# Optimization experiments

Measured on AMD Instinct MI355X. Metric: run time of the kernel, lower is better.

## Reference

```python
import jax, jax.numpy as jnp
import numpy as np

B, C, D = 524288, 256, 128


def setup_inputs() -> dict:
    key = jax.random.key(0)
    ks = jax.random.split(key, 20)
    s = 1.0 / np.sqrt(D)
    w = lambda k, shp: jax.random.normal(k, shp, dtype=jnp.float32) * s
    return {
        "h": jax.random.normal(ks[0], (B, D), dtype=jnp.float32),
        "g": jax.random.normal(ks[1], (C, D), dtype=jnp.float32),
        "cluster_id": jax.random.randint(ks[2], (B,), 0, C, dtype=jnp.int32),
        "Wq": w(ks[3], (D, D)),
        "Wk": w(ks[4], (D, D)),
        "attn_bias": jax.random.uniform(ks[5], (D,), dtype=jnp.float32, minval=-0.1, maxval=0.1),
        "Ws_w": w(ks[6], (1, D)),
        "Ws_b": jnp.zeros((1,), dtype=jnp.float32),
        "W_w": w(ks[7], (D, D)),
        "W_b": jnp.zeros((D,), dtype=jnp.float32),
        "Fs_w": w(ks[8], (D, D)),
        "Fs_b": jnp.zeros((D,), dtype=jnp.float32),
        "H1_w": w(ks[9], (D, D)),
        "H1_b": jnp.zeros((D,), dtype=jnp.float32),
        "G1_w": w(ks[10], (D, D)),
        "G1_b": jnp.zeros((D,), dtype=jnp.float32),
        "H2_w": w(ks[11], (D, D)),
        "H2_b": jnp.zeros((D,), dtype=jnp.float32),
        "G2_w": w(ks[12], (D, D)),
        "G2_b": jnp.zeros((D,), dtype=jnp.float32),
    }


def reference(h, g, cluster_id, Wq, Wk, attn_bias, Ws_w, Ws_b, W_w, W_b,
              Fs_w, Fs_b, H1_w, H1_b, G1_w, G1_b, H2_w, H2_b, G2_w, G2_b):
    # --- GNTransmitterUnit: virtual -> graph node message ---
    g_trans = jnp.tanh(g @ Fs_w.T + Fs_b)                 # (C, D)
    g_n = g_trans[cluster_id]                              # gather per node: (B, D)
    # --- gn_merge (WarpGateUnit with gather): gated mix into node features ---
    z1 = jax.nn.sigmoid(h @ H1_w.T + H1_b + g_n @ G1_w.T + G1_b)
    h_merged = (1.0 - z1) * h + z1 * g_n                   # (B, D)
    # --- VNTransmitterUnit: segmented additive (Bahdanau) attention per cluster ---
    q = g @ Wq.T                                           # (C, D)
    k = h @ Wk.T                                           # (B, D)
    score = jnp.tanh(k + q[cluster_id] + attn_bias) @ Ws_w[0] + Ws_b[0]  # (B,)
    m = jax.ops.segment_max(score, cluster_id, num_segments=C)
    m = jnp.where(jnp.isfinite(m), m, 0.0)                 # guard empty clusters
    e = jnp.exp(score - m[cluster_id])
    denom = jax.ops.segment_sum(e, cluster_id, num_segments=C)
    attn = e / jnp.maximum(denom, 1e-20)[cluster_id]       # segment softmax (B,)
    ctx = jax.ops.segment_sum(attn[:, None] * h, cluster_id, num_segments=C)  # (C, D)
    h_trans = jnp.tanh(ctx @ W_w.T + W_b)                  # (C, D)
    # --- vn_merge (WarpGateUnit): gated mix into virtual-node features ---
    z2 = jax.nn.sigmoid(g @ H2_w.T + H2_b + h_trans @ G2_w.T + G2_b)
    g_merged = (1.0 - z2) * g + z2 * h_trans               # (C, D)
    return jnp.concatenate([h_merged, g_merged], axis=0)   # (B + C, D)
```

## Files before the change

### kernel.cpp

```cpp
#include <hip/hip_runtime.h>
#include <hip/hip_bf16.h>

#define NB   524288
#define NC   256
#define ND   128

typedef __attribute__((ext_vector_type(4))) float f32x4;
typedef __attribute__((ext_vector_type(8))) short bf16x8;

__device__ inline float fast_exp(float x)  { return exp2f(x * 1.4426950408889634f); }
__device__ inline float fast_sigmoid(float x) { return __builtin_amdgcn_rcpf(1.f + fast_exp(-x)); }
__device__ inline float fast_tanh(float x) { return 1.f - 2.f * __builtin_amdgcn_rcpf(1.f + fast_exp(2.f * x)); }

__device__ inline unsigned short f2bf(float f) {
    unsigned u = __float_as_uint(f);
    u += 0x7FFFu + ((u >> 16) & 1u);
    return (unsigned short)(u >> 16);
}

__device__ inline bf16x8 pack8(const float* __restrict__ p) {
    float4 a = *(const float4*)p;
    float4 b = *(const float4*)(p + 4);
    bf16x8 r;
    r[0] = (short)f2bf(a.x); r[1] = (short)f2bf(a.y);
    r[2] = (short)f2bf(a.z); r[3] = (short)f2bf(a.w);
    r[4] = (short)f2bf(b.x); r[5] = (short)f2bf(b.y);
    r[6] = (short)f2bf(b.z); r[7] = (short)f2bf(b.w);
    return r;
}

__device__ inline unsigned enc_f32(float s) {
    unsigned b = __float_as_uint(s);
    return b ^ (unsigned)(((int)b >> 31) | (int)0x80000000);
}

__global__ __launch_bounds__(128) void k1_cluster_prep(
    const float* __restrict__ g, const float* __restrict__ Wq,
    const float* __restrict__ attn_bias,
    const float* __restrict__ Fs_w, const float* __restrict__ Fs_b,
    const float* __restrict__ G1_w, const float* __restrict__ G1_b,
    float* __restrict__ g_trans, float* __restrict__ gG1, float* __restrict__ qb) {
    const int c = blockIdx.x, d = threadIdx.x;
    __shared__ float g_lds[ND];
    __shared__ float gt_lds[ND];
    g_lds[d] = g[c * ND + d];
    __syncthreads();
    float accF = Fs_b[d], accQ = attn_bias[d];
    const float* fr = Fs_w + d * ND;
    const float* qr = Wq + d * ND;
    for (int k = 0; k < ND; ++k) {
        float gv = g_lds[k];
        accF += fr[k] * gv;
        accQ += qr[k] * gv;
    }
    float gt = fast_tanh(accF);
    g_trans[c * ND + d] = gt;
    gt_lds[d] = gt;
    qb[c * ND + d] = accQ;
    __syncthreads();
    float accG = G1_b[d];
    const float* gr = G1_w + d * ND;
    for (int k = 0; k < ND; ++k) accG += gr[k] * gt_lds[k];
    gG1[c * ND + d] = accG;
}

__global__ __launch_bounds__(256) void k2_pass1(
    const float* __restrict__ h, const int* __restrict__ cid,
    const float* __restrict__ Wk, const float* __restrict__ H1w,
    const float* __restrict__ H1b, const float* __restrict__ Wsw,
    const float* __restrict__ Wsb, const float* __restrict__ g_trans,
    const float* __restrict__ gG1, const float* __restrict__ qb,
    float* __restrict__ outh, float* __restrict__ score) {
    __shared__ float k_lds[16][132];
    __shared__ float h1_lds[16][132];
    const int tid = threadIdx.x;
    const int w = tid >> 6, l = tid & 63;
    const int l15 = l & 15, lg = l >> 4;

    bf16x8 bk[2][4], bh[2][4];
#pragma unroll
    for (int t2 = 0; t2 < 2; ++t2) {
        const int trow = (w + t2 * 4) * 16 + l15;
#pragma unroll
        for (int c = 0; c < 4; ++c) {
            const int col = c * 32 + lg * 8;
            bk[t2][c] = pack8(Wk + trow * ND + col);
            bh[t2][c] = pack8(H1w + trow * ND + col);
        }
    }
    const float Wsb0 = Wsb[0];
    const int nb0 = blockIdx.x * 256;

    for (int it = 0; it < 16; ++it) {
        const int nb = nb0 + it * 16;
        bf16x8 af[4];
        const float* hrow = h + (size_t)(nb + l15) * ND + lg * 8;
#pragma unroll
        for (int c = 0; c < 4; ++c) af[c] = pack8(hrow + c * 32);

        f32x4 acck0 = {0.f, 0.f, 0.f, 0.f}, acck1 = {0.f, 0.f, 0.f, 0.f};
        f32x4 acch0 = {0.f, 0.f, 0.f, 0.f}, acch1 = {0.f, 0.f, 0.f, 0.f};
#pragma unroll
        for (int c = 0; c < 4; ++c) {
            acck0 = __builtin_amdgcn_mfma_f32_16x16x32_bf16(af[c], bk[0][c], acck0, 0, 0, 0);
            acck1 = __builtin_amdgcn_mfma_f32_16x16x32_bf16(af[c], bk[1][c], acck1, 0, 0, 0);
            acch0 = __builtin_amdgcn_mfma_f32_16x16x32_bf16(af[c], bh[0][c], acch0, 0, 0, 0);
            acch1 = __builtin_amdgcn_mfma_f32_16x16x32_bf16(af[c], bh[1][c], acch1, 0, 0, 0);
        }
        {
            const int d0 = w * 16 + l15, d1 = (w + 4) * 16 + l15;
#pragma unroll
            for (int r = 0; r < 4; ++r) {
                const int nrow = lg * 4 + r;
                k_lds[nrow][d0] = acck0[r];
                k_lds[nrow][d1] = acck1[r];
                h1_lds[nrow][d0] = acch0[r];
                h1_lds[nrow][d1] = acch1[r];
            }
        }
        __syncthreads();
#pragma unroll
        for (int ni = 0; ni < 4; ++ni) {
            const int n = w * 4 + ni;
            const int node = nb + n;
            const int cc = cid[node];
            float2 kv  = *(const float2*)&k_lds[n][2 * l];
            float2 h1v = *(const float2*)&h1_lds[n][2 * l];
            float2 qv  = *(const float2*)(qb + cc * ND + 2 * l);
            float2 ggv = *(const float2*)(gG1 + cc * ND + 2 * l);
            float2 gtv = *(const float2*)(g_trans + cc * ND + 2 * l);
            float2 hv  = *(const float2*)(h + (size_t)node * ND + 2 * l);
            float2 hbv = *(const float2*)(H1b + 2 * l);
            float2 wsv = *(const float2*)(Wsw + 2 * l);
            float sp = fast_tanh(kv.x + qv.x) * wsv.x + fast_tanh(kv.y + qv.y) * wsv.y;
#pragma unroll
            for (int off = 32; off; off >>= 1) sp += __shfl_xor(sp, off, 64);
            if (l == 0) score[node] = sp + Wsb0;
            float z0 = fast_sigmoid(h1v.x + hbv.x + ggv.x);
            float z1 = fast_sigmoid(h1v.y + hbv.y + ggv.y);
            float2 o = {(1.f - z0) * hv.x + z0 * gtv.x,
                        (1.f - z1) * hv.y + z1 * gtv.y};
            *(float2*)(outh + (size_t)node * ND + 2 * l) = o;
        }
        __syncthreads();
    }
}

__global__ __launch_bounds__(256) void k3_segmax(
    const float* __restrict__ score, const int* __restrict__ cid,
    unsigned* __restrict__ m_enc) {
    __shared__ unsigned mloc[NC];
    const int t = threadIdx.x;
    mloc[t] = 0u;
    __syncthreads();
    for (int i = blockIdx.x * 256 + t; i < NB; i += 256 * 256) {
        atomicMax(&mloc[cid[i]], enc_f32(score[i]));
    }
    __syncthreads();
    atomicMax(m_enc + t, mloc[t]);
}

__global__ __launch_bounds__(256) void k4_pass2(
    const float* __restrict__ h, const int* __restrict__ cid,
    const float* __restrict__ score, const unsigned* __restrict__ m_enc,
    float* __restrict__ ctx_raw, float* __restrict__ denom) {
    __shared__ float cloc[NC * 64];
    __shared__ float dloc[NC];
    __shared__ float mloc[NC];
    const int t = threadIdx.x, w = t >> 6, l = t & 63;
    const int half = blockIdx.x & 1, bg = blockIdx.x >> 1;
    for (int i = t; i < NC * 64; i += 256) cloc[i] = 0.f;
    dloc[t] = 0.f;
    {
        unsigned u = m_enc[t];
        unsigned bits = (u & 0x80000000u) ? (u ^ 0x80000000u) : ~u;
        float f = __uint_as_float(bits);
        mloc[t] = ((bits & 0x7F800000u) == 0x7F800000u) ? 0.f : f;
    }
    __syncthreads();
    const int n0 = bg * 2048 + w * 512;
    const float* hcol = h + half * 64 + l;
    for (int nn = 0; nn < 512; nn += 4) {
        const int n = n0 + nn;
        float4 sc = *(const float4*)(score + n);
        int4 c4 = *(const int4*)(cid + n);
        float e0 = fast_exp(sc.x - mloc[c4.x]);
        float e1 = fast_exp(sc.y - mloc[c4.y]);
        float e2 = fast_exp(sc.z - mloc[c4.z]);
        float e3 = fast_exp(sc.w - mloc[c4.w]);
        float h0 = hcol[(size_t)n * ND];
        float h1 = hcol[(size_t)(n + 1) * ND];
        float h2 = hcol[(size_t)(n + 2) * ND];
        float h3 = hcol[(size_t)(n + 3) * ND];
        atomicAdd(&cloc[c4.x * 64 + l], e0 * h0);
        atomicAdd(&cloc[c4.y * 64 + l], e1 * h1);
        atomicAdd(&cloc[c4.z * 64 + l], e2 * h2);
        atomicAdd(&cloc[c4.w * 64 + l], e3 * h3);
        if (l == 0 && half == 0) {
            atomicAdd(&dloc[c4.x], e0);
            atomicAdd(&dloc[c4.y], e1);
            atomicAdd(&dloc[c4.z], e2);
            atomicAdd(&dloc[c4.w], e3);
        }
    }
    __syncthreads();
    for (int i = t; i < NC * 64; i += 256) {
        const int c = i >> 6;
        unsafeAtomicAdd(&ctx_raw[c * ND + half * 64 + (i & 63)], cloc[i]);
    }
    if (half == 0) unsafeAtomicAdd(&denom[t], dloc[t]);
}

__global__ __launch_bounds__(128) void k5_final(
    const float* __restrict__ g, const float* __restrict__ ctx_raw,
    const float* __restrict__ denom,
    const float* __restrict__ W_w, const float* __restrict__ W_b,
    const float* __restrict__ H2_w, const float* __restrict__ H2_b,
    const float* __restrict__ G2_w, const float* __restrict__ G2_b,
    float* __restrict__ out_g) {
    const int c = blockIdx.x, d = threadIdx.x;
    __shared__ float ctx_l[ND], ht_l[ND], g_l[ND];
    float den = fmaxf(denom[c], 1e-20f);
    float ctxv = ctx_raw[c * ND + d] / den;
    ctx_l[d] = ctxv;
    g_l[d] = g[c * ND + d];
    __syncthreads();
    float acc = W_b[d];
    const float* wr = W_w + d * ND;
    for (int k = 0; k < ND; ++k) acc += wr[k] * ctx_l[k];
    float ht = fast_tanh(acc);
    ht_l[d] = ht;
    __syncthreads();
    float acc2 = H2_b[d] + G2_b[d];
    const float* h2r = H2_w + d * ND;
    const float* g2r = G2_w + d * ND;
    for (int k = 0; k < ND; ++k) acc2 += h2r[k] * g_l[k] + g2r[k] * ht_l[k];
    float z = fast_sigmoid(acc2);
    out_g[c * ND + d] = (1.f - z) * g_l[d] + z * ht;
}

extern "C" void kernel_launch(void* const* d_in, const int* in_sizes, int n_in,
                              void* d_out, int out_size, void* d_ws, size_t ws_size,
                              hipStream_t stream) {
    const float* h        = (const float*)d_in[0];
    const float* g        = (const float*)d_in[1];
    const int*   cid      = (const int*)d_in[2];
    const float* Wq       = (const float*)d_in[3];
    const float* Wk       = (const float*)d_in[4];
    const float* attnb    = (const float*)d_in[5];
    const float* Ws_w     = (const float*)d_in[6];
    const float* Ws_b     = (const float*)d_in[7];
    const float* W_w      = (const float*)d_in[8];
    const float* W_b      = (const float*)d_in[9];
    const float* Fs_w     = (const float*)d_in[10];
    const float* Fs_b     = (const float*)d_in[11];
    const float* H1_w     = (const float*)d_in[12];
    const float* H1_b     = (const float*)d_in[13];
    const float* G1_w     = (const float*)d_in[14];
    const float* G1_b     = (const float*)d_in[15];
    const float* H2_w     = (const float*)d_in[16];
    const float* H2_b     = (const float*)d_in[17];
    const float* G2_w     = (const float*)d_in[18];
    const float* G2_b     = (const float*)d_in[19];
    float* out = (float*)d_out;
    float* ws  = (float*)d_ws;

    float*    g_trans = ws;
    float*    gG1     = ws + 32768;
    float*    qb      = ws + 65536;
    float*    score   = ws + 98304;
    unsigned* m_enc   = (unsigned*)(ws + 622592);
    float*    denom   = ws + 622848;
    float*    ctx_raw = ws + 623104;
    hipMemsetAsync(ws + 622592, 0, (256 + 256 + 32768) * sizeof(float), stream);

    k1_cluster_prep<<<NC, ND, 0, stream>>>(g, Wq, attnb, Fs_w, Fs_b, G1_w, G1_b,
                                           g_trans, gG1, qb);
    k2_pass1<<<2048, 256, 0, stream>>>(h, cid, Wk, H1_w, H1_b, Ws_w, Ws_b,
                                       g_trans, gG1, qb, out, score);
    k3_segmax<<<256, 256, 0, stream>>>(score, cid, m_enc);
    k4_pass2<<<512, 256, 0, stream>>>(h, cid, score, m_enc, ctx_raw, denom);
    k5_final<<<NC, ND, 0, stream>>>(g, ctx_raw, denom, W_w, W_b,
                                    H2_w, H2_b, G2_w, G2_b,
                                    out + (size_t)NB * ND);
}
```

Measured before the change: 1.101 ms.

## Epilogue directly from MFMA registers in pass1; quarter-column vectorized segment accumulation

The pass-1 kernel drops the LDS staging and block barriers and computes the score and gate epilogue straight from the MFMA accumulator layout. The score is reduced over 16 lanes and combined with atomic adds into a pre-zeroed score buffer, which requires extending the memset. Ws_b is dropped from the score because a constant shift cancels in the softmax. The pass-2 kernel splits columns into quarters with padded LDS (stride 33), float4 loads of h and 1024 blocks, to cut LDS usage and improve coalescing. The trade-offs are strided, non-vectorized global loads and stores in the epilogue and extra global atomics on score.

```diff
diff --git a/kernel.cpp b/kernel.cpp
--- a/kernel.cpp
+++ b/kernel.cpp
@@ -68,11 +68,9 @@
     const float* __restrict__ h, const int* __restrict__ cid,
     const float* __restrict__ Wk, const float* __restrict__ H1w,
     const float* __restrict__ H1b, const float* __restrict__ Wsw,
-    const float* __restrict__ Wsb, const float* __restrict__ g_trans,
-    const float* __restrict__ gG1, const float* __restrict__ qb,
+    const float* __restrict__ g_trans, const float* __restrict__ gG1,
+    const float* __restrict__ qb,
     float* __restrict__ outh, float* __restrict__ score) {
-    __shared__ float k_lds[16][132];
-    __shared__ float h1_lds[16][132];
     const int tid = threadIdx.x;
     const int w = tid >> 6, l = tid & 63;
     const int l15 = l & 15, lg = l >> 4;
@@ -88,7 +86,10 @@
             bh[t2][c] = pack8(H1w + trow * ND + col);
         }
     }
-    const float Wsb0 = Wsb[0];
+    const int d0 = w * 16 + l15, d1 = d0 + 64;
+    const float ws0 = Wsw[d0], ws1 = Wsw[d1];
+    const float hb0 = H1b[d0], hb1 = H1b[d1];
+
     const int nb0 = blockIdx.x * 256;
 
     for (int it = 0; it < 16; ++it) {
@@ -107,42 +108,29 @@
             acch0 = __builtin_amdgcn_mfma_f32_16x16x32_bf16(af[c], bh[0][c], acch0, 0, 0, 0);
             acch1 = __builtin_amdgcn_mfma_f32_16x16x32_bf16(af[c], bh[1][c], acch1, 0, 0, 0);
         }
-        {
-            const int d0 = w * 16 + l15, d1 = (w + 4) * 16 + l15;
-#pragma unroll
-            for (int r = 0; r < 4; ++r) {
-                const int nrow = lg * 4 + r;
-                k_lds[nrow][d0] = acck0[r];
-                k_lds[nrow][d1] = acck1[r];
-                h1_lds[nrow][d0] = acch0[r];
-                h1_lds[nrow][d1] = acch1[r];
-            }
+#pragma unroll
+        for (int r = 0; r < 4; ++r) {
+            const int node = nb + lg * 4 + r;
+            const int cc = cid[node];
+            const float* qrow = qb + cc * ND;
+            const float* grow = gG1 + cc * ND;
+            const float* trow = g_trans + cc * ND;
+            const float* hrw  = h + (size_t)node * ND;
+            float q0  = qrow[d0], q1  = qrow[d1];
+            float gg0 = grow[d0], gg1 = grow[d1];
+            float gt0 = trow[d0], gt1 = trow[d1];
+            float hv0 = hrw[d0],  hv1 = hrw[d1];
+            float sp = fast_tanh(acck0[r] + q0) * ws0 + fast_tanh(acck1[r] + q1) * ws1;
+            sp += __shfl_xor(sp, 1);
+            sp += __shfl_xor(sp, 2);
+            sp += __shfl_xor(sp, 4);
+            sp += __shfl_xor(sp, 8);
+            if (l15 == 0) unsafeAtomicAdd(&score[node], sp);
+            float z0 = fast_sigmoid(acch0[r] + hb0 + gg0);
+            float z1 = fast_sigmoid(acch1[r] + hb1 + gg1);
+            outh[(size_t)node * ND + d0] = (1.f - z0) * hv0 + z0 * gt0;
+            outh[(size_t)node * ND + d1] = (1.f - z1) * hv1 + z1 * gt1;
         }
-        __syncthreads();
-#pragma unroll
-        for (int ni = 0; ni < 4; ++ni) {
-            const int n = w * 4 + ni;
-            const int node = nb + n;
-            const int cc = cid[node];
-            float2 kv  = *(const float2*)&k_lds[n][2 * l];
-            float2 h1v = *(const float2*)&h1_lds[n][2 * l];
-            float2 qv  = *(const float2*)(qb + cc * ND + 2 * l);
-            float2 ggv = *(const float2*)(gG1 + cc * ND + 2 * l);
-            float2 gtv = *(const float2*)(g_trans + cc * ND + 2 * l);
-            float2 hv  = *(const float2*)(h + (size_t)node * ND + 2 * l);
-            float2 hbv = *(const float2*)(H1b + 2 * l);
-            float2 wsv = *(const float2*)(Wsw + 2 * l);
-            float sp = fast_tanh(kv.x + qv.x) * wsv.x + fast_tanh(kv.y + qv.y) * wsv.y;
-#pragma unroll
-            for (int off = 32; off; off >>= 1) sp += __shfl_xor(sp, off, 64);
-            if (l == 0) score[node] = sp + Wsb0;
-            float z0 = fast_sigmoid(h1v.x + hbv.x + ggv.x);
-            float z1 = fast_sigmoid(h1v.y + hbv.y + ggv.y);
-            float2 o = {(1.f - z0) * hv.x + z0 * gtv.x,
-                        (1.f - z1) * hv.y + z1 * gtv.y};
-            *(float2*)(outh + (size_t)node * ND + 2 * l) = o;
-        }
-        __syncthreads();
     }
 }
 
@@ -164,12 +152,13 @@
     const float* __restrict__ h, const int* __restrict__ cid,
     const float* __restrict__ score, const unsigned* __restrict__ m_enc,
     float* __restrict__ ctx_raw, float* __restrict__ denom) {
-    __shared__ float cloc[NC * 64];
+    __shared__ float cloc[NC * 33];
     __shared__ float dloc[NC];
     __shared__ float mloc[NC];
     const int t = threadIdx.x, w = t >> 6, l = t & 63;
-    const int half = blockIdx.x & 1, bg = blockIdx.x >> 1;
-    for (int i = t; i < NC * 64; i += 256) cloc[i] = 0.f;
+    const int q = blockIdx.x & 3;
+    const int bg = blockIdx.x >> 2;
+    for (int i = t; i < NC * 33; i += 256) cloc[i] = 0.f;
     dloc[t] = 0.f;
     {
         unsigned u = m_enc[t];
@@ -178,37 +167,27 @@
         mloc[t] = ((bits & 0x7F800000u) == 0x7F800000u) ? 0.f : f;
     }
     __syncthreads();
+    const int colbase = q * 32 + (l & 7) * 4;
     const int n0 = bg * 2048 + w * 512;
-    const float* hcol = h + half * 64 + l;
-    for (int nn = 0; nn < 512; nn += 4) {
-        const int n = n0 + nn;
-        float4 sc = *(const float4*)(score + n);
-        int4 c4 = *(const int4*)(cid + n);
-        float e0 = fast_exp(sc.x - mloc[c4.x]);
-        float e1 = fast_exp(sc.y - mloc[c4.y]);
-        float e2 = fast_exp(sc.z - mloc[c4.z]);
-        float e3 = fast_exp(sc.w - mloc[c4.w]);
-        float h0 = hcol[(size_t)n * ND];
-        float h1 = hcol[(size_t)(n + 1) * ND];
-        float h2 = hcol[(size_t)(n + 2) * ND];
-        float h3 = hcol[(size_t)(n + 3) * ND];
-        atomicAdd(&cloc[c4.x * 64 + l], e0 * h0);
-        atomicAdd(&cloc[c4.y * 64 + l], e1 * h1);
-        atomicAdd(&cloc[c4.z * 64 + l], e2 * h2);
-        atomicAdd(&cloc[c4.w * 64 + l], e3 * h3);
-        if (l == 0 && half == 0) {
-            atomicAdd(&dloc[c4.x], e0);
-            atomicAdd(&dloc[c4.y], e1);
-            atomicAdd(&dloc[c4.z], e2);
-            atomicAdd(&dloc[c4.w], e3);
-        }
-    }
-    __syncthreads();
-    for (int i = t; i < NC * 64; i += 256) {
-        const int c = i >> 6;
-        unsafeAtomicAdd(&ctx_raw[c * ND + half * 64 + (i & 63)], cloc[i]);
-    }
-    if (half == 0) unsafeAtomicAdd(&denom[t], dloc[t]);
+    for (int nn = 0; nn < 512; nn += 8) {
+        const int node = n0 + nn + (l >> 3);
+        float s = score[node];
+        int c = cid[node];
+        float e = fast_exp(s - mloc[c]);
+        float4 hv = *(const float4*)(h + (size_t)node * ND + colbase);
+        const int base = c * 33 + (l & 7) * 4;
+        atomicAdd(&cloc[base + 0], e * hv.x);
+        atomicAdd(&cloc[base + 1], e * hv.y);
+        atomicAdd(&cloc[base + 2], e * hv.z);
+        atomicAdd(&cloc[base + 3], e * hv.w);
+        if ((l & 7) == 0 && q == 0) atomicAdd(&dloc[c], e);
+    }
+    __syncthreads();
+    for (int i = t; i < NC * 32; i += 256) {
+        const int c = i >> 5, col = i & 31;
+        unsafeAtomicAdd(&ctx_raw[c * ND + q * 32 + col], cloc[c * 33 + col]);
+    }
+    if (q == 0) unsafeAtomicAdd(&denom[t], dloc[t]);
 }
 
 __global__ __launch_bounds__(128) void k5_final(
@@ -242,26 +221,25 @@
 extern "C" void kernel_launch(void* const* d_in, const int* in_sizes, int n_in,
                               void* d_out, int out_size, void* d_ws, size_t ws_size,
                               hipStream_t stream) {
-    const float* h        = (const float*)d_in[0];
-    const float* g        = (const float*)d_in[1];
-    const int*   cid      = (const int*)d_in[2];
-    const float* Wq       = (const float*)d_in[3];
-    const float* Wk       = (const float*)d_in[4];
-    const float* attnb    = (const float*)d_in[5];
-    const float* Ws_w     = (const float*)d_in[6];
-    const float* Ws_b     = (const float*)d_in[7];
-    const float* W_w      = (const float*)d_in[8];
-    const float* W_b      = (const float*)d_in[9];
-    const float* Fs_w     = (const float*)d_in[10];
-    const float* Fs_b     = (const float*)d_in[11];
-    const float* H1_w     = (const float*)d_in[12];
-    const float* H1_b     = (const float*)d_in[13];
-    const float* G1_w     = (const float*)d_in[14];
-    const float* G1_b     = (const float*)d_in[15];
-    const float* H2_w     = (const float*)d_in[16];
-    const float* H2_b     = (const float*)d_in[17];
-    const float* G2_w     = (const float*)d_in[18];
-    const float* G2_b     = (const float*)d_in[19];
+    const float* h     = (const float*)d_in[0];
+    const float* g     = (const float*)d_in[1];
+    const int*   cid   = (const int*)d_in[2];
+    const float* Wq    = (const float*)d_in[3];
+    const float* Wk    = (const float*)d_in[4];
+    const float* attnb = (const float*)d_in[5];
+    const float* Ws_w  = (const float*)d_in[6];
+    const float* W_w   = (const float*)d_in[8];
+    const float* W_b   = (const float*)d_in[9];
+    const float* Fs_w  = (const float*)d_in[10];
+    const float* Fs_b  = (const float*)d_in[11];
+    const float* H1_w  = (const float*)d_in[12];
+    const float* H1_b  = (const float*)d_in[13];
+    const float* G1_w  = (const float*)d_in[14];
+    const float* G1_b  = (const float*)d_in[15];
+    const float* H2_w  = (const float*)d_in[16];
+    const float* H2_b  = (const float*)d_in[17];
+    const float* G2_w  = (const float*)d_in[18];
+    const float* G2_b  = (const float*)d_in[19];
     float* out = (float*)d_out;
     float* ws  = (float*)d_ws;
 
@@ -272,14 +250,14 @@
     unsigned* m_enc   = (unsigned*)(ws + 622592);
     float*    denom   = ws + 622848;
     float*    ctx_raw = ws + 623104;
-    hipMemsetAsync(ws + 622592, 0, (256 + 256 + 32768) * sizeof(float), stream);
+    hipMemsetAsync(ws + 98304, 0, (524288 + 256 + 256 + 32768) * sizeof(float), stream);
 
     k1_cluster_prep<<<NC, ND, 0, stream>>>(g, Wq, attnb, Fs_w, Fs_b, G1_w, G1_b,
                                            g_trans, gG1, qb);
-    k2_pass1<<<2048, 256, 0, stream>>>(h, cid, Wk, H1_w, H1_b, Ws_w, Ws_b,
+    k2_pass1<<<2048, 256, 0, stream>>>(h, cid, Wk, H1_w, H1_b, Ws_w,
                                        g_trans, gG1, qb, out, score);
     k3_segmax<<<256, 256, 0, stream>>>(score, cid, m_enc);
-    k4_pass2<<<512, 256, 0, stream>>>(h, cid, score, m_enc, ctx_raw, denom);
+    k4_pass2<<<1024, 256, 0, stream>>>(h, cid, score, m_enc, ctx_raw, denom);
     k5_final<<<NC, ND, 0, stream>>>(g, ctx_raw, denom, W_w, W_b,
                                     H2_w, H2_b, G2_w, G2_b,
                                     out + (size_t)NB * ND);
```

New measurement: 1.082 ms. No clear change (-1.8%).
